# Kernel tuning notes

Measured on AMD Instinct MI355X. Metric: run time of the kernel, lower is better.

Reference implementation:

```python
import jax, jax.numpy as jnp
import numpy as np

N_NODES = 100000
N_EDGES = 1600000
D_IN = 128
D_OUT = 128


def setup_inputs() -> dict:
    key = jax.random.key(0)
    k1, k2, k3, k4 = jax.random.split(key, 4)
    feat = jax.random.normal(k1, (N_NODES, D_IN), dtype=jnp.float32)
    W1 = jax.random.normal(k2, (D_OUT, D_IN), dtype=jnp.float32) * (1.0 / np.sqrt(D_IN))
    src = jax.random.randint(k3, (N_EDGES,), 0, N_NODES, dtype=jnp.int32)
    # ensure every dst node has at least one in-edge (no empty segments, like a
    # DGL graph without isolated destination nodes)
    dst_rand = jax.random.randint(k4, (N_EDGES - N_NODES,), 0, N_NODES, dtype=jnp.int32)
    dst = jnp.concatenate([jnp.arange(N_NODES, dtype=jnp.int32), dst_rand])
    return {"feat": feat, "W1": W1, "src": src, "dst": dst}


def reference(feat, W1, src, dst):
    # nn.Linear(bias=False): h = feat @ W1.T   -> [N, D_OUT]
    norm_h = jnp.einsum("nd,od->no", feat, W1)
    # copy_u message + max reduce: segment-max of projected src feats onto dst
    msgs = norm_h[src]                                   # [E, D_OUT] gather
    h_N = jax.ops.segment_max(msgs, dst, num_segments=feat.shape[0])  # [N, D_OUT]
    # concat(feat_dst, h_N) along feature dim
    return jnp.concatenate([feat, h_N], axis=1)          # [N, D_IN + D_OUT]
```

## Files before the change

### kernel.cpp

```cpp
#include <hip/hip_runtime.h>
#include <hip/hip_bf16.h>
#include <cfloat>

typedef short bf16x8 __attribute__((ext_vector_type(8)));
typedef float f32x4 __attribute__((ext_vector_type(4)));

constexpr int NB2    = 1600;
constexpr int PCHUNK = 8192;
constexpr int BCAP2  = 2048;
constexpr int EREG2  = 8;

__device__ __forceinline__ unsigned short f32_to_bf16_rne(float f) {
    unsigned int u = __float_as_uint(f);
    u += 0x7fffu + ((u >> 16) & 1u);
    return (unsigned short)(u >> 16);
}
__device__ __forceinline__ float b2f(unsigned int w, int k) {
    return (float)((int)(w << (24 - 8 * k)) >> 24);
}

__global__ __launch_bounds__(256) void ka_gemm_hist_kernel(
    const float* __restrict__ feat, const float* __restrict__ W1,
    signed char* __restrict__ norm8, float* __restrict__ rowscale,
    float* __restrict__ out, const int* __restrict__ dst,
    unsigned short* __restrict__ chunkPre,
    int N, int E, int nb2, int nhist) {
    __shared__ __align__(16) char smem[32768];
    const int t = threadIdx.x;

    if ((int)blockIdx.x < nhist) {
        int* pkCnt = (int*)smem;
        for (int i = t; i < NB2 / 2; i += 256) pkCnt[i] = 0;
        __syncthreads();
        int c0 = blockIdx.x * PCHUNK;
#pragma unroll
        for (int j = 0; j < PCHUNK / 1024; ++j) {
            int i = c0 + (j * 256 + t) * 4;
            if (i + 3 < E) {
                int4 d4 = *(const int4*)(dst + i);
                atomicAdd(&pkCnt[(d4.x >> 6) >> 1], 1 << (((d4.x >> 6) & 1) << 4));
                atomicAdd(&pkCnt[(d4.y >> 6) >> 1], 1 << (((d4.y >> 6) & 1) << 4));
                atomicAdd(&pkCnt[(d4.z >> 6) >> 1], 1 << (((d4.z >> 6) & 1) << 4));
                atomicAdd(&pkCnt[(d4.w >> 6) >> 1], 1 << (((d4.w >> 6) & 1) << 4));
            } else if (i < E) {
                for (int k = i; k < E; ++k) {
                    int b = dst[k] >> 6;
                    atomicAdd(&pkCnt[b >> 1], 1 << ((b & 1) << 4));
                }
            }
        }
        __syncthreads();
        unsigned short* rowp = chunkPre + (size_t)blockIdx.x * NB2;
        for (int b = t; b < nb2; b += 256)
            rowp[b] = (unsigned short)((pkCnt[b >> 1] >> ((b & 1) << 4)) & 0xFFFF);
    } else {
        unsigned short* smW = (unsigned short*)smem;
#pragma unroll
        for (int i = 0; i < 8; ++i) {
            int f = i * 256 + t;
            int l = f & 63, kb = (f >> 6) & 3, ot = f >> 8;
            int wrow = ot * 16 + (l & 15);
            int k0 = kb * 32 + (l >> 4) * 8;
            const float* p = W1 + wrow * 128 + k0;
            float4 f0 = *(const float4*)p;
            float4 f1 = *(const float4*)(p + 4);
            union { unsigned short h[8]; uint4 v; } pk;
            pk.h[0] = f32_to_bf16_rne(f0.x); pk.h[1] = f32_to_bf16_rne(f0.y);
            pk.h[2] = f32_to_bf16_rne(f0.z); pk.h[3] = f32_to_bf16_rne(f0.w);
            pk.h[4] = f32_to_bf16_rne(f1.x); pk.h[5] = f32_to_bf16_rne(f1.y);
            pk.h[6] = f32_to_bf16_rne(f1.z); pk.h[7] = f32_to_bf16_rne(f1.w);
            *(uint4*)(smW + (size_t)f * 8) = pk.v;
        }

        const int bid = blockIdx.x - nhist;
        const int w = t >> 6;
        const int l = t & 63;
        const int brow0 = bid * 64;
        const int row = brow0 + w * 16 + (l & 15);
        const int kq = (l >> 4) * 8;
        const bool valid = row < N;

        bf16x8 a[4];
        const float* fr = feat + (size_t)row * 128;
        float* orow = out + (size_t)row * 256;
#pragma unroll
        for (int kb = 0; kb < 4; ++kb) {
            float4 f0 = make_float4(0.f, 0.f, 0.f, 0.f), f1 = f0;
            if (valid) {
                f0 = *(const float4*)(fr + kb * 32 + kq);
                f1 = *(const float4*)(fr + kb * 32 + kq + 4);
                *(float4*)(orow + kb * 32 + kq) = f0;
                *(float4*)(orow + kb * 32 + kq + 4) = f1;
            }
            bf16x8 av;
            av[0] = (short)f32_to_bf16_rne(f0.x); av[1] = (short)f32_to_bf16_rne(f0.y);
            av[2] = (short)f32_to_bf16_rne(f0.z); av[3] = (short)f32_to_bf16_rne(f0.w);
            av[4] = (short)f32_to_bf16_rne(f1.x); av[5] = (short)f32_to_bf16_rne(f1.y);
            av[6] = (short)f32_to_bf16_rne(f1.z); av[7] = (short)f32_to_bf16_rne(f1.w);
            a[kb] = av;
        }
        __syncthreads();

        const bf16x8* bfr = (const bf16x8*)smem;
        f32x4 zero = {0.f, 0.f, 0.f, 0.f};
        f32x4 acc[8];
#pragma unroll
        for (int ot = 0; ot < 8; ++ot) acc[ot] = zero;
#pragma unroll
        for (int ot = 0; ot < 8; ++ot) {
#pragma unroll
            for (int kb = 0; kb < 4; ++kb) {
                bf16x8 b = bfr[(ot * 4 + kb) * 64 + l];
                acc[ot] = __builtin_amdgcn_mfma_f32_16x16x32_bf16(a[kb], b, acc[ot], 0, 0, 0);
            }
        }

        const int r0 = w * 16 + (l >> 4) * 4;
        float inv[4], scl[4];
#pragma unroll
        for (int j = 0; j < 4; ++j) {
            float am = 0.f;
#pragma unroll
            for (int ot = 0; ot < 8; ++ot) am = fmaxf(am, __builtin_fabsf(acc[ot][j]));
#pragma unroll
            for (int d = 1; d < 16; d <<= 1) am = fmaxf(am, __shfl_xor(am, d, 64));
            am = fmaxf(am, 1e-30f);
            inv[j] = 127.0f / am;
            scl[j] = am * (1.0f / 127.0f);
        }
        if ((l & 15) == 0) {
#pragma unroll
            for (int j = 0; j < 4; ++j) {
                int grow = brow0 + r0 + j;
                if (grow < N) rowscale[grow] = scl[j];
            }
        }
        __syncthreads();

        char (*sm8)[144] = (char (*)[144])smem;
        const int c0 = l & 15;
#pragma unroll
        for (int ot = 0; ot < 8; ++ot)
#pragma unroll
            for (int j = 0; j < 4; ++j)
                sm8[r0 + j][ot * 16 + c0] = (char)(int)rintf(acc[ot][j] * inv[j]);
        __syncthreads();
#pragma unroll
        for (int i = 0; i < 2; ++i) {
            int idx = i * 256 + t;
            int r = idx >> 3, c = idx & 7;
            int grow = brow0 + r;
            if (grow < N) {
                uint4 v = *(const uint4*)&sm8[r][c * 16];
                *(uint4*)(norm8 + (size_t)grow * 128 + c * 16) = v;
            }
        }
    }
}

__global__ __launch_bounds__(256) void kb_scan_kernel(
    unsigned short* __restrict__ chunkPre, int* __restrict__ btot,
    int nchunks, int nb2) {
    int wid = blockIdx.x * 4 + (threadIdx.x >> 6);
    int lane = threadIdx.x & 63;
    if (wid >= nb2) return;
    int carry = 0;
    int rounds = (nchunks + 63) / 64;
    for (int r = 0; r < rounds; ++r) {
        int c = r * 64 + lane;
        int orig = (c < nchunks) ? (int)chunkPre[(size_t)c * NB2 + wid] : 0;
        int v = orig;
#pragma unroll
        for (int d = 1; d < 64; d <<= 1) {
            int x = __shfl_up(v, d, 64);
            if (lane >= d) v += x;
        }
        if (c < nchunks)
            chunkPre[(size_t)c * NB2 + wid] = (unsigned short)(carry + v - orig);
        carry += __shfl(v, 63, 64);
    }
    if (lane == 0) btot[wid] = carry;
}

__global__ __launch_bounds__(256) void kc_part_kernel(
    const int* __restrict__ src, const int* __restrict__ dst,
    const unsigned short* __restrict__ chunkPre, int* __restrict__ part,
    int E, int nb2) {
    __shared__ int gdst[NB2];
    __shared__ int pkLoc[NB2 / 2];
    const int t = threadIdx.x;
    for (int i = t; i < NB2 / 2; i += 256) pkLoc[i] = 0;
    const unsigned short* pre = chunkPre + (size_t)blockIdx.x * NB2;
    for (int b = t; b < nb2; b += 256) gdst[b] = b * BCAP2 + (int)pre[b];
    __syncthreads();

    int c0 = blockIdx.x * PCHUNK;
#pragma unroll
    for (int j = 0; j < PCHUNK / 1024; ++j) {
        int i = c0 + (j * 256 + t) * 4;
        if (i + 3 < E) {
            int4 d4 = *(const int4*)(dst + i);
            int4 s4 = *(const int4*)(src + i);
            int b, sh, old, slot;
            b = d4.x >> 6; sh = (b & 1) << 4;
            old = atomicAdd(&pkLoc[b >> 1], 1 << sh);
            slot = gdst[b] + ((old >> sh) & 0xFFFF);
            if (slot < ((b + 1) << 11)) part[slot] = s4.x | ((d4.x & 63) << 17);
            b = d4.y >> 6; sh = (b & 1) << 4;
            old = atomicAdd(&pkLoc[b >> 1], 1 << sh);
            slot = gdst[b] + ((old >> sh) & 0xFFFF);
            if (slot < ((b + 1) << 11)) part[slot] = s4.y | ((d4.y & 63) << 17);
            b = d4.z >> 6; sh = (b & 1) << 4;
            old = atomicAdd(&pkLoc[b >> 1], 1 << sh);
            slot = gdst[b] + ((old >> sh) & 0xFFFF);
            if (slot < ((b + 1) << 11)) part[slot] = s4.z | ((d4.z & 63) << 17);
            b = d4.w >> 6; sh = (b & 1) << 4;
            old = atomicAdd(&pkLoc[b >> 1], 1 << sh);
            slot = gdst[b] + ((old >> sh) & 0xFFFF);
            if (slot < ((b + 1) << 11)) part[slot] = s4.w | ((d4.w & 63) << 17);
        } else if (i < E) {
            for (int k = i; k < E; ++k) {
                int d = dst[k];
                int b = d >> 6, sh = (b & 1) << 4;
                int old = atomicAdd(&pkLoc[b >> 1], 1 << sh);
                int slot = gdst[b] + ((old >> sh) & 0xFFFF);
                if (slot < ((b + 1) << 11)) part[slot] = src[k] | ((d & 63) << 17);
            }
        }
    }
}

__global__ __launch_bounds__(256) void kd_maxpool_kernel(
    const signed char* __restrict__ norm8, const float* __restrict__ rowscale,
    const int* __restrict__ part, const int* __restrict__ btot,
    float* __restrict__ out, int N) {
    __shared__ int eoff[65];
    __shared__ int eloc[64];
    __shared__ int esrc[BCAP2];

    const int B = blockIdx.x;
    const int t = threadIdx.x;
    int cnt = btot[B];
    if (cnt > BCAP2) cnt = BCAP2;
    const int* p = part + (size_t)B * BCAP2;

    int ev[EREG2];
#pragma unroll
    for (int j = 0; j < EREG2; ++j) {
        int i = j * 256 + t;
        ev[j] = (i < cnt) ? p[i] : -1;
    }

    if (t < 64) eloc[t] = 0;
    __syncthreads();
#pragma unroll
    for (int j = 0; j < EREG2; ++j) {
        int v = ev[j];
        if (v >= 0) atomicAdd(&eloc[(v >> 17) & 63], 1);
    }
    __syncthreads();
    if (t < 64) {
        int v = eloc[t];
        int sc = v;
#pragma unroll
        for (int d = 1; d < 64; d <<= 1) {
            int x = __shfl_up(sc, d, 64);
            if (t >= d) sc += x;
        }
        int excl = sc - v;
        eoff[t] = excl;
        eloc[t] = excl;
        if (t == 63) eoff[64] = sc;
    }
    __syncthreads();
#pragma unroll
    for (int j = 0; j < EREG2; ++j) {
        int v = ev[j];
        if (v >= 0) esrc[atomicAdd(&eloc[(v >> 17) & 63], 1)] = v & 0x1FFFF;
    }
    __syncthreads();

    int qw = t >> 4;
    int ln = t & 15;
    const size_t colb = (size_t)ln * 8;
    for (int dl = qw; dl < 64; dl += 16) {
        int node = B * 64 + dl;
        if (node >= N) break;
        int si = eoff[dl], se = eoff[dl + 1];
        float a0 = -FLT_MAX, a1 = -FLT_MAX, a2 = -FLT_MAX, a3 = -FLT_MAX;
        float a4 = -FLT_MAX, a5 = -FLT_MAX, a6 = -FLT_MAX, a7 = -FLT_MAX;
        float b0 = -FLT_MAX, b1 = -FLT_MAX, b2 = -FLT_MAX, b3 = -FLT_MAX;
        float b4 = -FLT_MAX, b5 = -FLT_MAX, b6 = -FLT_MAX, b7 = -FLT_MAX;
        float c0 = -FLT_MAX, c1 = -FLT_MAX, c2 = -FLT_MAX, c3 = -FLT_MAX;
        float c4 = -FLT_MAX, c5 = -FLT_MAX, c6 = -FLT_MAX, c7 = -FLT_MAX;
        float d0 = -FLT_MAX, d1 = -FLT_MAX, d2 = -FLT_MAX, d3 = -FLT_MAX;
        float d4 = -FLT_MAX, d5 = -FLT_MAX, d6 = -FLT_MAX, d7 = -FLT_MAX;
        int i = si;
        for (; i + 3 < se; i += 4) {
            int s1 = esrc[i], s2 = esrc[i + 1], s3 = esrc[i + 2], s4 = esrc[i + 3];
            uint2 wA = *(const uint2*)(norm8 + (size_t)s1 * 128 + colb);
            uint2 wB = *(const uint2*)(norm8 + (size_t)s2 * 128 + colb);
            uint2 wC = *(const uint2*)(norm8 + (size_t)s3 * 128 + colb);
            uint2 wD = *(const uint2*)(norm8 + (size_t)s4 * 128 + colb);
            float sA = rowscale[s1], sB = rowscale[s2];
            float sC = rowscale[s3], sD = rowscale[s4];
            a0 = fmaxf(a0, b2f(wA.x, 0) * sA); a1 = fmaxf(a1, b2f(wA.x, 1) * sA);
            a2 = fmaxf(a2, b2f(wA.x, 2) * sA); a3 = fmaxf(a3, b2f(wA.x, 3) * sA);
            a4 = fmaxf(a4, b2f(wA.y, 0) * sA); a5 = fmaxf(a5, b2f(wA.y, 1) * sA);
            a6 = fmaxf(a6, b2f(wA.y, 2) * sA); a7 = fmaxf(a7, b2f(wA.y, 3) * sA);
            b0 = fmaxf(b0, b2f(wB.x, 0) * sB); b1 = fmaxf(b1, b2f(wB.x, 1) * sB);
            b2 = fmaxf(b2, b2f(wB.x, 2) * sB); b3 = fmaxf(b3, b2f(wB.x, 3) * sB);
            b4 = fmaxf(b4, b2f(wB.y, 0) * sB); b5 = fmaxf(b5, b2f(wB.y, 1) * sB);
            b6 = fmaxf(b6, b2f(wB.y, 2) * sB); b7 = fmaxf(b7, b2f(wB.y, 3) * sB);
            c0 = fmaxf(c0, b2f(wC.x, 0) * sC); c1 = fmaxf(c1, b2f(wC.x, 1) * sC);
            c2 = fmaxf(c2, b2f(wC.x, 2) * sC); c3 = fmaxf(c3, b2f(wC.x, 3) * sC);
            c4 = fmaxf(c4, b2f(wC.y, 0) * sC); c5 = fmaxf(c5, b2f(wC.y, 1) * sC);
            c6 = fmaxf(c6, b2f(wC.y, 2) * sC); c7 = fmaxf(c7, b2f(wC.y, 3) * sC);
            d0 = fmaxf(d0, b2f(wD.x, 0) * sD); d1 = fmaxf(d1, b2f(wD.x, 1) * sD);
            d2 = fmaxf(d2, b2f(wD.x, 2) * sD); d3 = fmaxf(d3, b2f(wD.x, 3) * sD);
            d4 = fmaxf(d4, b2f(wD.y, 0) * sD); d5 = fmaxf(d5, b2f(wD.y, 1) * sD);
            d6 = fmaxf(d6, b2f(wD.y, 2) * sD); d7 = fmaxf(d7, b2f(wD.y, 3) * sD);
        }
        for (; i < se; ++i) {
            int s1 = esrc[i];
            uint2 wA = *(const uint2*)(norm8 + (size_t)s1 * 128 + colb);
            float sA = rowscale[s1];
            a0 = fmaxf(a0, b2f(wA.x, 0) * sA); a1 = fmaxf(a1, b2f(wA.x, 1) * sA);
            a2 = fmaxf(a2, b2f(wA.x, 2) * sA); a3 = fmaxf(a3, b2f(wA.x, 3) * sA);
            a4 = fmaxf(a4, b2f(wA.y, 0) * sA); a5 = fmaxf(a5, b2f(wA.y, 1) * sA);
            a6 = fmaxf(a6, b2f(wA.y, 2) * sA); a7 = fmaxf(a7, b2f(wA.y, 3) * sA);
        }
        a0 = fmaxf(a0, b0); a1 = fmaxf(a1, b1); a2 = fmaxf(a2, b2); a3 = fmaxf(a3, b3);
        a4 = fmaxf(a4, b4); a5 = fmaxf(a5, b5); a6 = fmaxf(a6, b6); a7 = fmaxf(a7, b7);
        c0 = fmaxf(c0, d0); c1 = fmaxf(c1, d1); c2 = fmaxf(c2, d2); c3 = fmaxf(c3, d3);
        c4 = fmaxf(c4, d4); c5 = fmaxf(c5, d5); c6 = fmaxf(c6, d6); c7 = fmaxf(c7, d7);
        a0 = fmaxf(a0, c0); a1 = fmaxf(a1, c1); a2 = fmaxf(a2, c2); a3 = fmaxf(a3, c3);
        a4 = fmaxf(a4, c4); a5 = fmaxf(a5, c5); a6 = fmaxf(a6, c6); a7 = fmaxf(a7, c7);
        float* op = out + (size_t)node * 256 + 128 + colb;
        *(float4*)op       = make_float4(a0, a1, a2, a3);
        *(float4*)(op + 4) = make_float4(a4, a5, a6, a7);
    }
}

extern "C" void kernel_launch(void* const* d_in, const int* in_sizes, int n_in,
                              void* d_out, int out_size, void* d_ws, size_t ws_size,
                              hipStream_t stream) {
    const float* feat = (const float*)d_in[0];
    const float* W1   = (const float*)d_in[1];
    const int*   src  = (const int*)d_in[2];
    const int*   dst  = (const int*)d_in[3];
    float* out = (float*)d_out;

    const int N = in_sizes[0] / 128;
    const int E = in_sizes[2];
    const int nb2 = (N + 63) >> 6;
    const int nchunks = (E + PCHUNK - 1) / PCHUNK;
    const int gemmBlocks = (N + 63) / 64;

    char* wsp = (char*)d_ws;
    size_t o = 0;
    signed char* norm8 = (signed char*)(wsp + o);
    o += ((size_t)N * 128 + 255) & ~(size_t)255;
    float* rowscale = (float*)(wsp + o);
    o += ((size_t)N * 4 + 255) & ~(size_t)255;
    int* part = (int*)(wsp + o);
    o += ((size_t)NB2 * BCAP2 * 4 + 255) & ~(size_t)255;
    unsigned short* chunkPre = (unsigned short*)(wsp + o);
    o += ((size_t)nchunks * NB2 * 2 + 255) & ~(size_t)255;
    int* btot = (int*)(wsp + o);  o += NB2 * 4;

    ka_gemm_hist_kernel<<<nchunks + gemmBlocks, 256, 0, stream>>>(
        feat, W1, norm8, rowscale, out, dst, chunkPre, N, E, nb2, nchunks);
    kb_scan_kernel<<<(nb2 + 3) / 4, 256, 0, stream>>>(chunkPre, btot, nchunks, nb2);
    kc_part_kernel<<<nchunks, 256, 0, stream>>>(src, dst, chunkPre, part, E, nb2);
    kd_maxpool_kernel<<<nb2, 256, 0, stream>>>(norm8, rowscale, part, btot, out, N);
}
```

Baseline: 108.4 us.

## Move GEMM into partition kernel and precompute bf16 W1 fragments once

The GEMM blocks move out of the first launch, where they ran alongside the dst histogram, and into the third launch, where they run alongside the edge-partition scatter. The first kernel now also converts W1 to bf16 MFMA fragment layout once into a workspace buffer. Each GEMM block then copies the ready fragments into shared memory instead of converting W1 itself. The intent is to shrink the histogram and scan critical path and to balance work across launches, at the cost of an extra small global buffer and a larger third launch.

After: 106.6 us. No clear change (-1.7%).

```diff
diff --git a/kernel.cpp b/kernel.cpp
--- a/kernel.cpp
+++ b/kernel.cpp
@@ -19,146 +19,60 @@
     return (float)((int)(w << (24 - 8 * k)) >> 24);
 }
 
-__global__ __launch_bounds__(256) void ka_gemm_hist_kernel(
-    const float* __restrict__ feat, const float* __restrict__ W1,
-    signed char* __restrict__ norm8, float* __restrict__ rowscale,
-    float* __restrict__ out, const int* __restrict__ dst,
-    unsigned short* __restrict__ chunkPre,
-    int N, int E, int nb2, int nhist) {
-    __shared__ __align__(16) char smem[32768];
+__global__ __launch_bounds__(256) void k1_prep_hist_kernel(
+    const float* __restrict__ W1, unsigned short* __restrict__ w1frag,
+    const int* __restrict__ dst, unsigned short* __restrict__ chunkPre,
+    int E, int nb2) {
+    __shared__ int pkCnt[NB2 / 2];
     const int t = threadIdx.x;
 
-    if ((int)blockIdx.x < nhist) {
-        int* pkCnt = (int*)smem;
-        for (int i = t; i < NB2 / 2; i += 256) pkCnt[i] = 0;
-        __syncthreads();
-        int c0 = blockIdx.x * PCHUNK;
-#pragma unroll
-        for (int j = 0; j < PCHUNK / 1024; ++j) {
-            int i = c0 + (j * 256 + t) * 4;
-            if (i + 3 < E) {
-                int4 d4 = *(const int4*)(dst + i);
-                atomicAdd(&pkCnt[(d4.x >> 6) >> 1], 1 << (((d4.x >> 6) & 1) << 4));
-                atomicAdd(&pkCnt[(d4.y >> 6) >> 1], 1 << (((d4.y >> 6) & 1) << 4));
-                atomicAdd(&pkCnt[(d4.z >> 6) >> 1], 1 << (((d4.z >> 6) & 1) << 4));
-                atomicAdd(&pkCnt[(d4.w >> 6) >> 1], 1 << (((d4.w >> 6) & 1) << 4));
-            } else if (i < E) {
-                for (int k = i; k < E; ++k) {
-                    int b = dst[k] >> 6;
-                    atomicAdd(&pkCnt[b >> 1], 1 << ((b & 1) << 4));
-                }
-            }
-        }
-        __syncthreads();
-        unsigned short* rowp = chunkPre + (size_t)blockIdx.x * NB2;
-        for (int b = t; b < nb2; b += 256)
-            rowp[b] = (unsigned short)((pkCnt[b >> 1] >> ((b & 1) << 4)) & 0xFFFF);
-    } else {
-        unsigned short* smW = (unsigned short*)smem;
-#pragma unroll
-        for (int i = 0; i < 8; ++i) {
-            int f = i * 256 + t;
-            int l = f & 63, kb = (f >> 6) & 3, ot = f >> 8;
-            int wrow = ot * 16 + (l & 15);
-            int k0 = kb * 32 + (l >> 4) * 8;
-            const float* p = W1 + wrow * 128 + k0;
-            float4 f0 = *(const float4*)p;
-            float4 f1 = *(const float4*)(p + 4);
-            union { unsigned short h[8]; uint4 v; } pk;
-            pk.h[0] = f32_to_bf16_rne(f0.x); pk.h[1] = f32_to_bf16_rne(f0.y);
-            pk.h[2] = f32_to_bf16_rne(f0.z); pk.h[3] = f32_to_bf16_rne(f0.w);
-            pk.h[4] = f32_to_bf16_rne(f1.x); pk.h[5] = f32_to_bf16_rne(f1.y);
-            pk.h[6] = f32_to_bf16_rne(f1.z); pk.h[7] = f32_to_bf16_rne(f1.w);
-            *(uint4*)(smW + (size_t)f * 8) = pk.v;
-        }
-
-        const int bid = blockIdx.x - nhist;
-        const int w = t >> 6;
-        const int l = t & 63;
-        const int brow0 = bid * 64;
-        const int row = brow0 + w * 16 + (l & 15);
-        const int kq = (l >> 4) * 8;
-        const bool valid = row < N;
-
-        bf16x8 a[4];
-        const float* fr = feat + (size_t)row * 128;
-        float* orow = out + (size_t)row * 256;
-#pragma unroll
-        for (int kb = 0; kb < 4; ++kb) {
-            float4 f0 = make_float4(0.f, 0.f, 0.f, 0.f), f1 = f0;
-            if (valid) {
-                f0 = *(const float4*)(fr + kb * 32 + kq);
-                f1 = *(const float4*)(fr + kb * 32 + kq + 4);
-                *(float4*)(orow + kb * 32 + kq) = f0;
-                *(float4*)(orow + kb * 32 + kq + 4) = f1;
-            }
-            bf16x8 av;
-            av[0] = (short)f32_to_bf16_rne(f0.x); av[1] = (short)f32_to_bf16_rne(f0.y);
-            av[2] = (short)f32_to_bf16_rne(f0.z); av[3] = (short)f32_to_bf16_rne(f0.w);
-            av[4] = (short)f32_to_bf16_rne(f1.x); av[5] = (short)f32_to_bf16_rne(f1.y);
-            av[6] = (short)f32_to_bf16_rne(f1.z); av[7] = (short)f32_to_bf16_rne(f1.w);
-            a[kb] = av;
-        }
-        __syncthreads();
-
-        const bf16x8* bfr = (const bf16x8*)smem;
-        f32x4 zero = {0.f, 0.f, 0.f, 0.f};
-        f32x4 acc[8];
-#pragma unroll
-        for (int ot = 0; ot < 8; ++ot) acc[ot] = zero;
-#pragma unroll
-        for (int ot = 0; ot < 8; ++ot) {
-#pragma unroll
-            for (int kb = 0; kb < 4; ++kb) {
-                bf16x8 b = bfr[(ot * 4 + kb) * 64 + l];
-                acc[ot] = __builtin_amdgcn_mfma_f32_16x16x32_bf16(a[kb], b, acc[ot], 0, 0, 0);
-            }
-        }
-
-        const int r0 = w * 16 + (l >> 4) * 4;
-        float inv[4], scl[4];
-#pragma unroll
-        for (int j = 0; j < 4; ++j) {
-            float am = 0.f;
-#pragma unroll
-            for (int ot = 0; ot < 8; ++ot) am = fmaxf(am, __builtin_fabsf(acc[ot][j]));
-#pragma unroll
-            for (int d = 1; d < 16; d <<= 1) am = fmaxf(am, __shfl_xor(am, d, 64));
-            am = fmaxf(am, 1e-30f);
-            inv[j] = 127.0f / am;
-            scl[j] = am * (1.0f / 127.0f);
-        }
-        if ((l & 15) == 0) {
-#pragma unroll
-            for (int j = 0; j < 4; ++j) {
-                int grow = brow0 + r0 + j;
-                if (grow < N) rowscale[grow] = scl[j];
-            }
-        }
-        __syncthreads();
-
-        char (*sm8)[144] = (char (*)[144])smem;
-        const int c0 = l & 15;
-#pragma unroll
-        for (int ot = 0; ot < 8; ++ot)
-#pragma unroll
-            for (int j = 0; j < 4; ++j)
-                sm8[r0 + j][ot * 16 + c0] = (char)(int)rintf(acc[ot][j] * inv[j]);
-        __syncthreads();
-#pragma unroll
-        for (int i = 0; i < 2; ++i) {
-            int idx = i * 256 + t;
-            int r = idx >> 3, c = idx & 7;
-            int grow = brow0 + r;
-            if (grow < N) {
-                uint4 v = *(const uint4*)&sm8[r][c * 16];
-                *(uint4*)(norm8 + (size_t)grow * 128 + c * 16) = v;
-            }
-        }
-    }
-}
-
-__global__ __launch_bounds__(256) void kb_scan_kernel(
+    if ((int)blockIdx.x < 8) {
+        int g = blockIdx.x * 256 + t;
+        if (g >= 2048) return;
+        int l  = g & 63;
+        int kb = (g >> 6) & 3;
+        int ot = g >> 8;
+        int row = ot * 16 + (l & 15);
+        int k0  = kb * 32 + (l >> 4) * 8;
+        const float* p = W1 + row * 128 + k0;
+        float4 f0 = *(const float4*)p;
+        float4 f1 = *(const float4*)(p + 4);
+        union { unsigned short h[8]; uint4 v; } pk;
+        pk.h[0] = f32_to_bf16_rne(f0.x); pk.h[1] = f32_to_bf16_rne(f0.y);
+        pk.h[2] = f32_to_bf16_rne(f0.z); pk.h[3] = f32_to_bf16_rne(f0.w);
+        pk.h[4] = f32_to_bf16_rne(f1.x); pk.h[5] = f32_to_bf16_rne(f1.y);
+        pk.h[6] = f32_to_bf16_rne(f1.z); pk.h[7] = f32_to_bf16_rne(f1.w);
+        *(uint4*)(w1frag + (size_t)g * 8) = pk.v;
+        return;
+    }
+
+    const int c = blockIdx.x - 8;
+    for (int i = t; i < NB2 / 2; i += 256) pkCnt[i] = 0;
+    __syncthreads();
+    int c0 = c * PCHUNK;
+#pragma unroll
+    for (int j = 0; j < PCHUNK / 1024; ++j) {
+        int i = c0 + (j * 256 + t) * 4;
+        if (i + 3 < E) {
+            int4 d4 = *(const int4*)(dst + i);
+            atomicAdd(&pkCnt[(d4.x >> 6) >> 1], 1 << (((d4.x >> 6) & 1) << 4));
+            atomicAdd(&pkCnt[(d4.y >> 6) >> 1], 1 << (((d4.y >> 6) & 1) << 4));
+            atomicAdd(&pkCnt[(d4.z >> 6) >> 1], 1 << (((d4.z >> 6) & 1) << 4));
+            atomicAdd(&pkCnt[(d4.w >> 6) >> 1], 1 << (((d4.w >> 6) & 1) << 4));
+        } else if (i < E) {
+            for (int k = i; k < E; ++k) {
+                int b = dst[k] >> 6;
+                atomicAdd(&pkCnt[b >> 1], 1 << ((b & 1) << 4));
+            }
+        }
+    }
+    __syncthreads();
+    unsigned short* rowp = chunkPre + (size_t)c * NB2;
+    for (int b = t; b < nb2; b += 256)
+        rowp[b] = (unsigned short)((pkCnt[b >> 1] >> ((b & 1) << 4)) & 0xFFFF);
+}
+
+__global__ __launch_bounds__(256) void k2_scan_kernel(
     unsigned short* __restrict__ chunkPre, int* __restrict__ btot,
     int nchunks, int nb2) {
     int wid = blockIdx.x * 4 + (threadIdx.x >> 6);
@@ -182,55 +96,151 @@
     if (lane == 0) btot[wid] = carry;
 }
 
-__global__ __launch_bounds__(256) void kc_part_kernel(
+__global__ __launch_bounds__(256) void k3_part_gemm_kernel(
+    const float* __restrict__ feat, const unsigned short* __restrict__ w1frag,
+    signed char* __restrict__ norm8, float* __restrict__ rowscale,
+    float* __restrict__ out,
     const int* __restrict__ src, const int* __restrict__ dst,
     const unsigned short* __restrict__ chunkPre, int* __restrict__ part,
-    int E, int nb2) {
-    __shared__ int gdst[NB2];
-    __shared__ int pkLoc[NB2 / 2];
+    int N, int E, int nb2, int partBlocks) {
+    __shared__ __align__(16) char smem[32768];
     const int t = threadIdx.x;
-    for (int i = t; i < NB2 / 2; i += 256) pkLoc[i] = 0;
-    const unsigned short* pre = chunkPre + (size_t)blockIdx.x * NB2;
-    for (int b = t; b < nb2; b += 256) gdst[b] = b * BCAP2 + (int)pre[b];
-    __syncthreads();
-
-    int c0 = blockIdx.x * PCHUNK;
-#pragma unroll
-    for (int j = 0; j < PCHUNK / 1024; ++j) {
-        int i = c0 + (j * 256 + t) * 4;
-        if (i + 3 < E) {
-            int4 d4 = *(const int4*)(dst + i);
-            int4 s4 = *(const int4*)(src + i);
-            int b, sh, old, slot;
-            b = d4.x >> 6; sh = (b & 1) << 4;
-            old = atomicAdd(&pkLoc[b >> 1], 1 << sh);
-            slot = gdst[b] + ((old >> sh) & 0xFFFF);
-            if (slot < ((b + 1) << 11)) part[slot] = s4.x | ((d4.x & 63) << 17);
-            b = d4.y >> 6; sh = (b & 1) << 4;
-            old = atomicAdd(&pkLoc[b >> 1], 1 << sh);
-            slot = gdst[b] + ((old >> sh) & 0xFFFF);
-            if (slot < ((b + 1) << 11)) part[slot] = s4.y | ((d4.y & 63) << 17);
-            b = d4.z >> 6; sh = (b & 1) << 4;
-            old = atomicAdd(&pkLoc[b >> 1], 1 << sh);
-            slot = gdst[b] + ((old >> sh) & 0xFFFF);
-            if (slot < ((b + 1) << 11)) part[slot] = s4.z | ((d4.z & 63) << 17);
-            b = d4.w >> 6; sh = (b & 1) << 4;
-            old = atomicAdd(&pkLoc[b >> 1], 1 << sh);
-            slot = gdst[b] + ((old >> sh) & 0xFFFF);
-            if (slot < ((b + 1) << 11)) part[slot] = s4.w | ((d4.w & 63) << 17);
-        } else if (i < E) {
-            for (int k = i; k < E; ++k) {
-                int d = dst[k];
-                int b = d >> 6, sh = (b & 1) << 4;
-                int old = atomicAdd(&pkLoc[b >> 1], 1 << sh);
-                int slot = gdst[b] + ((old >> sh) & 0xFFFF);
-                if (slot < ((b + 1) << 11)) part[slot] = src[k] | ((d & 63) << 17);
-            }
-        }
-    }
-}
-
-__global__ __launch_bounds__(256) void kd_maxpool_kernel(
+
+    if ((int)blockIdx.x < partBlocks) {
+        int* gdst  = (int*)smem;
+        int* pkLoc = gdst + NB2;
+        for (int i = t; i < NB2 / 2; i += 256) pkLoc[i] = 0;
+        const unsigned short* pre = chunkPre + (size_t)blockIdx.x * NB2;
+        for (int b = t; b < nb2; b += 256) gdst[b] = b * BCAP2 + (int)pre[b];
+        __syncthreads();
+
+        int c0 = blockIdx.x * PCHUNK;
+#pragma unroll
+        for (int j = 0; j < PCHUNK / 1024; ++j) {
+            int i = c0 + (j * 256 + t) * 4;
+            if (i + 3 < E) {
+                int4 d4 = *(const int4*)(dst + i);
+                int4 s4 = *(const int4*)(src + i);
+                int b, sh, old, slot;
+                b = d4.x >> 6; sh = (b & 1) << 4;
+                old = atomicAdd(&pkLoc[b >> 1], 1 << sh);
+                slot = gdst[b] + ((old >> sh) & 0xFFFF);
+                if (slot < ((b + 1) << 11)) part[slot] = s4.x | ((d4.x & 63) << 17);
+                b = d4.y >> 6; sh = (b & 1) << 4;
+                old = atomicAdd(&pkLoc[b >> 1], 1 << sh);
+                slot = gdst[b] + ((old >> sh) & 0xFFFF);
+                if (slot < ((b + 1) << 11)) part[slot] = s4.y | ((d4.y & 63) << 17);
+                b = d4.z >> 6; sh = (b & 1) << 4;
+                old = atomicAdd(&pkLoc[b >> 1], 1 << sh);
+                slot = gdst[b] + ((old >> sh) & 0xFFFF);
+                if (slot < ((b + 1) << 11)) part[slot] = s4.z | ((d4.z & 63) << 17);
+                b = d4.w >> 6; sh = (b & 1) << 4;
+                old = atomicAdd(&pkLoc[b >> 1], 1 << sh);
+                slot = gdst[b] + ((old >> sh) & 0xFFFF);
+                if (slot < ((b + 1) << 11)) part[slot] = s4.w | ((d4.w & 63) << 17);
+            } else if (i < E) {
+                for (int k = i; k < E; ++k) {
+                    int d = dst[k];
+                    int b = d >> 6, sh = (b & 1) << 4;
+                    int old = atomicAdd(&pkLoc[b >> 1], 1 << sh);
+                    int slot = gdst[b] + ((old >> sh) & 0xFFFF);
+                    if (slot < ((b + 1) << 11)) part[slot] = src[k] | ((d & 63) << 17);
+                }
+            }
+        }
+    } else {
+        uint4* smW = (uint4*)smem;
+        const uint4* gw = (const uint4*)w1frag;
+#pragma unroll
+        for (int i = 0; i < 8; ++i) smW[i * 256 + t] = gw[i * 256 + t];
+
+        const int bid = blockIdx.x - partBlocks;
+        const int w = t >> 6;
+        const int l = t & 63;
+        const int brow0 = bid * 64;
+        const int row = brow0 + w * 16 + (l & 15);
+        const int kq = (l >> 4) * 8;
+        const bool valid = row < N;
+
+        bf16x8 a[4];
+        const float* fr = feat + (size_t)row * 128;
+        float* orow = out + (size_t)row * 256;
+#pragma unroll
+        for (int kb = 0; kb < 4; ++kb) {
+            float4 f0 = make_float4(0.f, 0.f, 0.f, 0.f), f1 = f0;
+            if (valid) {
+                f0 = *(const float4*)(fr + kb * 32 + kq);
+                f1 = *(const float4*)(fr + kb * 32 + kq + 4);
+                *(float4*)(orow + kb * 32 + kq) = f0;
+                *(float4*)(orow + kb * 32 + kq + 4) = f1;
+            }
+            bf16x8 av;
+            av[0] = (short)f32_to_bf16_rne(f0.x); av[1] = (short)f32_to_bf16_rne(f0.y);
+            av[2] = (short)f32_to_bf16_rne(f0.z); av[3] = (short)f32_to_bf16_rne(f0.w);
+            av[4] = (short)f32_to_bf16_rne(f1.x); av[5] = (short)f32_to_bf16_rne(f1.y);
+            av[6] = (short)f32_to_bf16_rne(f1.z); av[7] = (short)f32_to_bf16_rne(f1.w);
+            a[kb] = av;
+        }
+        __syncthreads();
+
+        const bf16x8* bfr = (const bf16x8*)smem;
+        f32x4 zero = {0.f, 0.f, 0.f, 0.f};
+        f32x4 acc[8];
+#pragma unroll
+        for (int ot = 0; ot < 8; ++ot) acc[ot] = zero;
+#pragma unroll
+        for (int ot = 0; ot < 8; ++ot) {
+#pragma unroll
+            for (int kb = 0; kb < 4; ++kb) {
+                bf16x8 b = bfr[(ot * 4 + kb) * 64 + l];
+                acc[ot] = __builtin_amdgcn_mfma_f32_16x16x32_bf16(a[kb], b, acc[ot], 0, 0, 0);
+            }
+        }
+
+        const int r0 = w * 16 + (l >> 4) * 4;
+        float inv[4], scl[4];
+#pragma unroll
+        for (int j = 0; j < 4; ++j) {
+            float am = 0.f;
+#pragma unroll
+            for (int ot = 0; ot < 8; ++ot) am = fmaxf(am, __builtin_fabsf(acc[ot][j]));
+#pragma unroll
+            for (int d = 1; d < 16; d <<= 1) am = fmaxf(am, __shfl_xor(am, d, 64));
+            am = fmaxf(am, 1e-30f);
+            inv[j] = 127.0f / am;
+            scl[j] = am * (1.0f / 127.0f);
+        }
+        if ((l & 15) == 0) {
+#pragma unroll
+            for (int j = 0; j < 4; ++j) {
+                int grow = brow0 + r0 + j;
+                if (grow < N) rowscale[grow] = scl[j];
+            }
+        }
+        __syncthreads();
+
+        char (*sm8)[144] = (char (*)[144])smem;
+        const int c0 = l & 15;
+#pragma unroll
+        for (int ot = 0; ot < 8; ++ot)
+#pragma unroll
+            for (int j = 0; j < 4; ++j)
+                sm8[r0 + j][ot * 16 + c0] = (char)(int)rintf(acc[ot][j] * inv[j]);
+        __syncthreads();
+#pragma unroll
+        for (int i = 0; i < 2; ++i) {
+            int idx = i * 256 + t;
+            int r = idx >> 3, c = idx & 7;
+            int grow = brow0 + r;
+            if (grow < N) {
+                uint4 v = *(const uint4*)&sm8[r][c * 16];
+                *(uint4*)(norm8 + (size_t)grow * 128 + c * 16) = v;
+            }
+        }
+    }
+}
+
+__global__ __launch_bounds__(256) void k4_maxpool_kernel(
     const signed char* __restrict__ norm8, const float* __restrict__ rowscale,
     const int* __restrict__ part, const int* __restrict__ btot,
     float* __restrict__ out, int N) {
@@ -368,10 +378,14 @@
     unsigned short* chunkPre = (unsigned short*)(wsp + o);
     o += ((size_t)nchunks * NB2 * 2 + 255) & ~(size_t)255;
     int* btot = (int*)(wsp + o);  o += NB2 * 4;
-
-    ka_gemm_hist_kernel<<<nchunks + gemmBlocks, 256, 0, stream>>>(
-        feat, W1, norm8, rowscale, out, dst, chunkPre, N, E, nb2, nchunks);
-    kb_scan_kernel<<<(nb2 + 3) / 4, 256, 0, stream>>>(chunkPre, btot, nchunks, nb2);
-    kc_part_kernel<<<nchunks, 256, 0, stream>>>(src, dst, chunkPre, part, E, nb2);
-    kd_maxpool_kernel<<<nb2, 256, 0, stream>>>(norm8, rowscale, part, btot, out, N);
-}
+    unsigned short* w1frag = (unsigned short*)(wsp + o);
+    o += 2048 * 8 * 2;
+
+    k1_prep_hist_kernel<<<8 + nchunks, 256, 0, stream>>>(
+        W1, w1frag, dst, chunkPre, E, nb2);
+    k2_scan_kernel<<<(nb2 + 3) / 4, 256, 0, stream>>>(chunkPre, btot, nchunks, nb2);
+    k3_part_gemm_kernel<<<nchunks + gemmBlocks, 256, 0, stream>>>(
+        feat, w1frag, norm8, rowscale, out, src, dst, chunkPre, part,
+        N, E, nb2, nchunks);
+    k4_maxpool_kernel<<<nb2, 256, 0, stream>>>(norm8, rowscale, part, btot, out, N);
+}
```

## Partition edges locally per chunk and gather runs in maxpool, dropping scan kernels

Applied to the files above, without the earlier changes.

Each chunk block now builds its own histogram, does a local scan, and sorts its edges by 128-node bucket in shared memory. It writes the chunk's edges contiguously to `part` along with a per-chunk offset row. The maxpool kernel, now one 512-thread block per 128 nodes, reads each chunk's run for its bucket and prefix-sums the run lengths itself. This removes the separate global scan and scatter kernels, two launches in total, and replaces the scattered global writes with coalesced ones. The cost is that the maxpool blocks read many small runs, about 196 per bucket, and use larger shared buffers.

New measurement: 95.83 us (median of 2 runs). 1.13x faster.

```diff
diff --git a/kernel.cpp b/kernel.cpp
--- a/kernel.cpp
+++ b/kernel.cpp
@@ -5,10 +5,11 @@
 typedef short bf16x8 __attribute__((ext_vector_type(8)));
 typedef float f32x4 __attribute__((ext_vector_type(4)));
 
-constexpr int NB2    = 1600;
-constexpr int PCHUNK = 8192;
-constexpr int BCAP2  = 2048;
-constexpr int EREG2  = 8;
+constexpr int NB_PAD  = 800;
+constexpr int PCHUNK  = 8192;
+constexpr int NCH_MAX = 200;
+constexpr int OFFROW  = 804;
+constexpr int BCAPM   = 4096;
 
 __device__ __forceinline__ unsigned short f32_to_bf16_rne(float f) {
     unsigned int u = __float_as_uint(f);
@@ -19,40 +20,108 @@
     return (float)((int)(w << (24 - 8 * k)) >> 24);
 }
 
-__global__ __launch_bounds__(256) void ka_gemm_hist_kernel(
+__global__ __launch_bounds__(256) void ka_part_gemm_kernel(
     const float* __restrict__ feat, const float* __restrict__ W1,
     signed char* __restrict__ norm8, float* __restrict__ rowscale,
-    float* __restrict__ out, const int* __restrict__ dst,
-    unsigned short* __restrict__ chunkPre,
-    int N, int E, int nb2, int nhist) {
-    __shared__ __align__(16) char smem[32768];
+    float* __restrict__ out,
+    const int* __restrict__ src, const int* __restrict__ dst,
+    int* __restrict__ part, unsigned short* __restrict__ offRow,
+    int N, int E, int nb, int partBlocks) {
+    __shared__ __align__(16) char smem[38912];
     const int t = threadIdx.x;
 
-    if ((int)blockIdx.x < nhist) {
-        int* pkCnt = (int*)smem;
-        for (int i = t; i < NB2 / 2; i += 256) pkCnt[i] = 0;
-        __syncthreads();
-        int c0 = blockIdx.x * PCHUNK;
+    if ((int)blockIdx.x < partBlocks) {
+        int* stage   = (int*)smem;
+        int* pkCnt   = stage + PCHUNK;
+        int* pkOff   = pkCnt + 400;
+        int* pkLoc   = pkOff + 400;
+        int* partial = pkLoc + 400;
+
+        const int c0 = blockIdx.x * PCHUNK;
+        const int n  = (E - c0 < PCHUNK) ? (E - c0) : PCHUNK;
+
+        for (int i = t; i < 400; i += 256) pkCnt[i] = 0;
+        __syncthreads();
+
 #pragma unroll
         for (int j = 0; j < PCHUNK / 1024; ++j) {
-            int i = c0 + (j * 256 + t) * 4;
-            if (i + 3 < E) {
-                int4 d4 = *(const int4*)(dst + i);
-                atomicAdd(&pkCnt[(d4.x >> 6) >> 1], 1 << (((d4.x >> 6) & 1) << 4));
-                atomicAdd(&pkCnt[(d4.y >> 6) >> 1], 1 << (((d4.y >> 6) & 1) << 4));
-                atomicAdd(&pkCnt[(d4.z >> 6) >> 1], 1 << (((d4.z >> 6) & 1) << 4));
-                atomicAdd(&pkCnt[(d4.w >> 6) >> 1], 1 << (((d4.w >> 6) & 1) << 4));
-            } else if (i < E) {
-                for (int k = i; k < E; ++k) {
-                    int b = dst[k] >> 6;
+            int i = (j * 256 + t) * 4;
+            if (i + 3 < n) {
+                int4 d4 = *(const int4*)(dst + c0 + i);
+                atomicAdd(&pkCnt[(d4.x >> 7) >> 1], 1 << (((d4.x >> 7) & 1) << 4));
+                atomicAdd(&pkCnt[(d4.y >> 7) >> 1], 1 << (((d4.y >> 7) & 1) << 4));
+                atomicAdd(&pkCnt[(d4.z >> 7) >> 1], 1 << (((d4.z >> 7) & 1) << 4));
+                atomicAdd(&pkCnt[(d4.w >> 7) >> 1], 1 << (((d4.w >> 7) & 1) << 4));
+            } else if (i < n) {
+                for (int k = i; k < n; ++k) {
+                    int b = dst[c0 + k] >> 7;
                     atomicAdd(&pkCnt[b >> 1], 1 << ((b & 1) << 4));
                 }
             }
         }
         __syncthreads();
-        unsigned short* rowp = chunkPre + (size_t)blockIdx.x * NB2;
-        for (int b = t; b < nb2; b += 256)
-            rowp[b] = (unsigned short)((pkCnt[b >> 1] >> ((b & 1) << 4)) & 0xFFFF);
+
+        {
+            int w0 = 0, w1 = 0;
+            if (t < 200) { w0 = pkCnt[2 * t]; w1 = pkCnt[2 * t + 1]; }
+            int c0_ = w0 & 0xFFFF, c1_ = (w0 >> 16) & 0xFFFF;
+            int c2_ = w1 & 0xFFFF, c3_ = (w1 >> 16) & 0xFFFF;
+            partial[t] = c0_ + c1_ + c2_ + c3_;
+            __syncthreads();
+            for (int d = 1; d < 256; d <<= 1) {
+                int x = (t >= d) ? partial[t - d] : 0;
+                __syncthreads();
+                if (t >= d) partial[t] += x;
+                __syncthreads();
+            }
+            if (t < 200) {
+                int run = t ? partial[t - 1] : 0;
+                int o0 = run, o1 = o0 + c0_, o2 = o1 + c1_, o3 = o2 + c2_;
+                pkOff[2 * t]     = o0 | (o1 << 16);
+                pkOff[2 * t + 1] = o2 | (o3 << 16);
+                pkLoc[2 * t]     = o0 | (o1 << 16);
+                pkLoc[2 * t + 1] = o2 | (o3 << 16);
+            }
+        }
+        __syncthreads();
+
+#pragma unroll
+        for (int j = 0; j < PCHUNK / 1024; ++j) {
+            int i = (j * 256 + t) * 4;
+            if (i + 3 < n) {
+                int4 d4 = *(const int4*)(dst + c0 + i);
+                int4 s4 = *(const int4*)(src + c0 + i);
+                int b, sh, old;
+                b = d4.x >> 7; sh = (b & 1) << 4;
+                old = atomicAdd(&pkLoc[b >> 1], 1 << sh);
+                stage[(old >> sh) & 0xFFFF] = s4.x | ((d4.x & 127) << 17);
+                b = d4.y >> 7; sh = (b & 1) << 4;
+                old = atomicAdd(&pkLoc[b >> 1], 1 << sh);
+                stage[(old >> sh) & 0xFFFF] = s4.y | ((d4.y & 127) << 17);
+                b = d4.z >> 7; sh = (b & 1) << 4;
+                old = atomicAdd(&pkLoc[b >> 1], 1 << sh);
+                stage[(old >> sh) & 0xFFFF] = s4.z | ((d4.z & 127) << 17);
+                b = d4.w >> 7; sh = (b & 1) << 4;
+                old = atomicAdd(&pkLoc[b >> 1], 1 << sh);
+                stage[(old >> sh) & 0xFFFF] = s4.w | ((d4.w & 127) << 17);
+            } else if (i < n) {
+                for (int k = i; k < n; ++k) {
+                    int d = dst[c0 + k];
+                    int b = d >> 7, sh = (b & 1) << 4;
+                    int old = atomicAdd(&pkLoc[b >> 1], 1 << sh);
+                    stage[(old >> sh) & 0xFFFF] = src[c0 + k] | ((d & 127) << 17);
+                }
+            }
+        }
+        __syncthreads();
+
+        for (int i = t * 4; i < n; i += 1024) {
+            if (i + 3 < n) *(int4*)(part + c0 + i) = *(const int4*)(stage + i);
+            else for (int k = i; k < n; ++k) part[c0 + k] = stage[k];
+        }
+        unsigned short* orow = offRow + (size_t)blockIdx.x * OFFROW;
+        for (int b = t; b <= nb; b += 256)
+            orow[b] = (unsigned short)((pkOff[b >> 1] >> ((b & 1) << 4)) & 0xFFFF);
     } else {
         unsigned short* smW = (unsigned short*)smem;
 #pragma unroll
@@ -72,7 +141,7 @@
             *(uint4*)(smW + (size_t)f * 8) = pk.v;
         }
 
-        const int bid = blockIdx.x - nhist;
+        const int bid = blockIdx.x - partBlocks;
         const int w = t >> 6;
         const int l = t & 63;
         const int brow0 = bid * 64;
@@ -82,15 +151,15 @@
 
         bf16x8 a[4];
         const float* fr = feat + (size_t)row * 128;
-        float* orow = out + (size_t)row * 256;
+        float* orow_ = out + (size_t)row * 256;
 #pragma unroll
         for (int kb = 0; kb < 4; ++kb) {
             float4 f0 = make_float4(0.f, 0.f, 0.f, 0.f), f1 = f0;
             if (valid) {
                 f0 = *(const float4*)(fr + kb * 32 + kq);
                 f1 = *(const float4*)(fr + kb * 32 + kq + 4);
-                *(float4*)(orow + kb * 32 + kq) = f0;
-                *(float4*)(orow + kb * 32 + kq + 4) = f1;
+                *(float4*)(orow_ + kb * 32 + kq) = f0;
+                *(float4*)(orow_ + kb * 32 + kq + 4) = f1;
             }
             bf16x8 av;
             av[0] = (short)f32_to_bf16_rne(f0.x); av[1] = (short)f32_to_bf16_rne(f0.y);
@@ -158,135 +227,96 @@
     }
 }
 
-__global__ __launch_bounds__(256) void kb_scan_kernel(
-    unsigned short* __restrict__ chunkPre, int* __restrict__ btot,
-    int nchunks, int nb2) {
-    int wid = blockIdx.x * 4 + (threadIdx.x >> 6);
-    int lane = threadIdx.x & 63;
-    if (wid >= nb2) return;
-    int carry = 0;
-    int rounds = (nchunks + 63) / 64;
-    for (int r = 0; r < rounds; ++r) {
-        int c = r * 64 + lane;
-        int orig = (c < nchunks) ? (int)chunkPre[(size_t)c * NB2 + wid] : 0;
-        int v = orig;
-#pragma unroll
-        for (int d = 1; d < 64; d <<= 1) {
-            int x = __shfl_up(v, d, 64);
-            if (lane >= d) v += x;
-        }
-        if (c < nchunks)
-            chunkPre[(size_t)c * NB2 + wid] = (unsigned short)(carry + v - orig);
-        carry += __shfl(v, 63, 64);
-    }
-    if (lane == 0) btot[wid] = carry;
-}
-
-__global__ __launch_bounds__(256) void kc_part_kernel(
-    const int* __restrict__ src, const int* __restrict__ dst,
-    const unsigned short* __restrict__ chunkPre, int* __restrict__ part,
-    int E, int nb2) {
-    __shared__ int gdst[NB2];
-    __shared__ int pkLoc[NB2 / 2];
-    const int t = threadIdx.x;
-    for (int i = t; i < NB2 / 2; i += 256) pkLoc[i] = 0;
-    const unsigned short* pre = chunkPre + (size_t)blockIdx.x * NB2;
-    for (int b = t; b < nb2; b += 256) gdst[b] = b * BCAP2 + (int)pre[b];
-    __syncthreads();
-
-    int c0 = blockIdx.x * PCHUNK;
-#pragma unroll
-    for (int j = 0; j < PCHUNK / 1024; ++j) {
-        int i = c0 + (j * 256 + t) * 4;
-        if (i + 3 < E) {
-            int4 d4 = *(const int4*)(dst + i);
-            int4 s4 = *(const int4*)(src + i);
-            int b, sh, old, slot;
-            b = d4.x >> 6; sh = (b & 1) << 4;
-            old = atomicAdd(&pkLoc[b >> 1], 1 << sh);
-            slot = gdst[b] + ((old >> sh) & 0xFFFF);
-            if (slot < ((b + 1) << 11)) part[slot] = s4.x | ((d4.x & 63) << 17);
-            b = d4.y >> 6; sh = (b & 1) << 4;
-            old = atomicAdd(&pkLoc[b >> 1], 1 << sh);
-            slot = gdst[b] + ((old >> sh) & 0xFFFF);
-            if (slot < ((b + 1) << 11)) part[slot] = s4.y | ((d4.y & 63) << 17);
-            b = d4.z >> 6; sh = (b & 1) << 4;
-            old = atomicAdd(&pkLoc[b >> 1], 1 << sh);
-            slot = gdst[b] + ((old >> sh) & 0xFFFF);
-            if (slot < ((b + 1) << 11)) part[slot] = s4.z | ((d4.z & 63) << 17);
-            b = d4.w >> 6; sh = (b & 1) << 4;
-            old = atomicAdd(&pkLoc[b >> 1], 1 << sh);
-            slot = gdst[b] + ((old >> sh) & 0xFFFF);
-            if (slot < ((b + 1) << 11)) part[slot] = s4.w | ((d4.w & 63) << 17);
-        } else if (i < E) {
-            for (int k = i; k < E; ++k) {
-                int d = dst[k];
-                int b = d >> 6, sh = (b & 1) << 4;
-                int old = atomicAdd(&pkLoc[b >> 1], 1 << sh);
-                int slot = gdst[b] + ((old >> sh) & 0xFFFF);
-                if (slot < ((b + 1) << 11)) part[slot] = src[k] | ((d & 63) << 17);
-            }
-        }
-    }
-}
-
-__global__ __launch_bounds__(256) void kd_maxpool_kernel(
+__global__ __launch_bounds__(512) void kb_maxpool_kernel(
     const signed char* __restrict__ norm8, const float* __restrict__ rowscale,
-    const int* __restrict__ part, const int* __restrict__ btot,
-    float* __restrict__ out, int N) {
-    __shared__ int eoff[65];
-    __shared__ int eloc[64];
-    __shared__ int esrc[BCAP2];
+    const int* __restrict__ part, const unsigned short* __restrict__ offRow,
+    float* __restrict__ out, int N, int nch) {
+    __shared__ int eraw[BCAPM];
+    __shared__ int esrc[BCAPM];
+    __shared__ int runs_s[NCH_MAX];
+    __shared__ int rlen[NCH_MAX + 1];
+    __shared__ int eoff[129];
+    __shared__ int eloc[128];
+    __shared__ int s128[128];
 
     const int B = blockIdx.x;
     const int t = threadIdx.x;
-    int cnt = btot[B];
-    if (cnt > BCAP2) cnt = BCAP2;
-    const int* p = part + (size_t)B * BCAP2;
-
-    int ev[EREG2];
-#pragma unroll
-    for (int j = 0; j < EREG2; ++j) {
-        int i = j * 256 + t;
-        ev[j] = (i < cnt) ? p[i] : -1;
-    }
-
-    if (t < 64) eloc[t] = 0;
-    __syncthreads();
-#pragma unroll
-    for (int j = 0; j < EREG2; ++j) {
-        int v = ev[j];
-        if (v >= 0) atomicAdd(&eloc[(v >> 17) & 63], 1);
+
+    for (int c = t; c < nch; c += 512) {
+        const unsigned short* orow = offRow + (size_t)c * OFFROW;
+        int s = orow[B];
+        int e = orow[B + 1];
+        runs_s[c] = s;
+        rlen[c] = e - s;
     }
     __syncthreads();
     if (t < 64) {
-        int v = eloc[t];
-        int sc = v;
-#pragma unroll
-        for (int d = 1; d < 64; d <<= 1) {
-            int x = __shfl_up(sc, d, 64);
-            if (t >= d) sc += x;
-        }
-        int excl = sc - v;
-        eoff[t] = excl;
-        eloc[t] = excl;
-        if (t == 63) eoff[64] = sc;
-    }
-    __syncthreads();
-#pragma unroll
-    for (int j = 0; j < EREG2; ++j) {
-        int v = ev[j];
-        if (v >= 0) esrc[atomicAdd(&eloc[(v >> 17) & 63], 1)] = v & 0x1FFFF;
+        int carry = 0;
+        int rounds = (nch + 63) / 64;
+        for (int r = 0; r < rounds; ++r) {
+            int c = r * 64 + t;
+            int orig = (c < nch) ? rlen[c] : 0;
+            int v = orig;
+#pragma unroll
+            for (int d = 1; d < 64; d <<= 1) {
+                int x = __shfl_up(v, d, 64);
+                if (t >= d) v += x;
+            }
+            if (c < nch) rlen[c] = carry + v - orig;
+            carry += __shfl(v, 63, 64);
+        }
+        if (t == 0) rlen[nch] = carry;
+    }
+    __syncthreads();
+    int cnt = rlen[nch];
+    if (cnt > BCAPM) cnt = BCAPM;
+
+    {
+        int g = t >> 4, ln = t & 15;
+        for (int c = g; c < nch; c += 32) {
+            int s = runs_s[c], d0 = rlen[c], l = rlen[c + 1] - rlen[c];
+            const int* gp = part + (size_t)c * PCHUNK + s;
+            for (int i = ln; i < l; i += 16) {
+                int d = d0 + i;
+                if (d < BCAPM) eraw[d] = gp[i];
+            }
+        }
+    }
+    if (t < 128) eloc[t] = 0;
+    __syncthreads();
+
+    for (int i = t; i < cnt; i += 512) atomicAdd(&eloc[eraw[i] >> 17], 1);
+    __syncthreads();
+    if (t < 128) s128[t] = eloc[t];
+    __syncthreads();
+    for (int d = 1; d < 128; d <<= 1) {
+        int x = 0;
+        if (t < 128 && t >= d) x = s128[t - d];
+        __syncthreads();
+        if (t < 128 && t >= d) s128[t] += x;
+        __syncthreads();
+    }
+    if (t < 128) {
+        int e = t ? s128[t - 1] : 0;
+        eoff[t] = e;
+        eloc[t] = e;
+    }
+    if (t == 0) eoff[128] = cnt;
+    __syncthreads();
+    for (int i = t; i < cnt; i += 512) {
+        int v = eraw[i];
+        esrc[atomicAdd(&eloc[v >> 17], 1)] = v & 0x1FFFF;
     }
     __syncthreads();
 
     int qw = t >> 4;
     int ln = t & 15;
     const size_t colb = (size_t)ln * 8;
-    for (int dl = qw; dl < 64; dl += 16) {
-        int node = B * 64 + dl;
+    for (int dl = qw; dl < 128; dl += 32) {
+        int node = (B << 7) + dl;
         if (node >= N) break;
         int si = eoff[dl], se = eoff[dl + 1];
+        if (se > BCAPM) se = BCAPM;
         float a0 = -FLT_MAX, a1 = -FLT_MAX, a2 = -FLT_MAX, a3 = -FLT_MAX;
         float a4 = -FLT_MAX, a5 = -FLT_MAX, a6 = -FLT_MAX, a7 = -FLT_MAX;
         float b0 = -FLT_MAX, b1 = -FLT_MAX, b2 = -FLT_MAX, b3 = -FLT_MAX;
@@ -353,7 +383,7 @@
 
     const int N = in_sizes[0] / 128;
     const int E = in_sizes[2];
-    const int nb2 = (N + 63) >> 6;
+    const int nb = (N + 127) >> 7;
     const int nchunks = (E + PCHUNK - 1) / PCHUNK;
     const int gemmBlocks = (N + 63) / 64;
 
@@ -364,14 +394,13 @@
     float* rowscale = (float*)(wsp + o);
     o += ((size_t)N * 4 + 255) & ~(size_t)255;
     int* part = (int*)(wsp + o);
-    o += ((size_t)NB2 * BCAP2 * 4 + 255) & ~(size_t)255;
-    unsigned short* chunkPre = (unsigned short*)(wsp + o);
-    o += ((size_t)nchunks * NB2 * 2 + 255) & ~(size_t)255;
-    int* btot = (int*)(wsp + o);  o += NB2 * 4;
-
-    ka_gemm_hist_kernel<<<nchunks + gemmBlocks, 256, 0, stream>>>(
-        feat, W1, norm8, rowscale, out, dst, chunkPre, N, E, nb2, nchunks);
-    kb_scan_kernel<<<(nb2 + 3) / 4, 256, 0, stream>>>(chunkPre, btot, nchunks, nb2);
-    kc_part_kernel<<<nchunks, 256, 0, stream>>>(src, dst, chunkPre, part, E, nb2);
-    kd_maxpool_kernel<<<nb2, 256, 0, stream>>>(norm8, rowscale, part, btot, out, N);
+    o += ((size_t)E * 4 + 255) & ~(size_t)255;
+    unsigned short* offRow = (unsigned short*)(wsp + o);
+    o += ((size_t)nchunks * OFFROW * 2 + 255) & ~(size_t)255;
+
+    ka_part_gemm_kernel<<<nchunks + gemmBlocks, 256, 0, stream>>>(
+        feat, W1, norm8, rowscale, out, src, dst, part, offRow,
+        N, E, nb, nchunks);
+    kb_maxpool_kernel<<<nb, 512, 0, stream>>>(
+        norm8, rowscale, part, offRow, out, N, nchunks);
 }
```
